# Kernel optimization log

Measured on AMD Instinct MI355X. Metric: run time of the kernel, lower is better.

Reference implementation:

```python
import jax, jax.numpy as jnp
import numpy as np

D_MODEL = 512
N_HEADS = 8
Q_SEQ_LEN = 1024
KV_SEQ_LEN = 1024
N_MODES = 64
D_HEAD = D_MODEL // N_HEADS

# FEDformer frequency_modes (deterministic/lowest branch): lowest n_modes freqs
Q_MODES = np.arange(min(N_MODES, Q_SEQ_LEN // 2))
KV_MODES = np.arange(min(N_MODES, KV_SEQ_LEN // 2))


def setup_inputs() -> dict:
    key = jax.random.key(0)
    kq, kk, kv, kwr, kwi = jax.random.split(key, 5)
    B = 8
    scale = 1.0 / (D_MODEL * D_MODEL)
    return {
        "query": jax.random.normal(kq, (B, N_HEADS, Q_SEQ_LEN, D_HEAD), jnp.float32),
        "key": jax.random.normal(kk, (B, N_HEADS, KV_SEQ_LEN, D_HEAD), jnp.float32),
        "value": jax.random.normal(kv, (B, N_HEADS, KV_SEQ_LEN, D_HEAD), jnp.float32),
        "weights_re": scale * jax.random.uniform(kwr, (N_HEADS, D_HEAD, D_HEAD, len(Q_MODES)), jnp.float32),
        "weights_im": scale * jax.random.uniform(kwi, (N_HEADS, D_HEAD, D_HEAD, len(Q_MODES)), jnp.float32),
    }


def reference(query, key, value, weights_re, weights_im):
    # value is accepted but unused by the original forward (FEA-f variant).
    B, H, L, D = query.shape
    q_modes = jnp.asarray(Q_MODES)
    kv_modes = jnp.asarray(KV_MODES)

    # [B,H,D,L] -> rfft along time -> gather selected frequency modes
    q_fft = jnp.fft.rfft(jnp.swapaxes(query, -2, -1), axis=-1)   # [B,H,D,L//2+1]
    k_fft = jnp.fft.rfft(jnp.swapaxes(key, -2, -1), axis=-1)     # [B,H,D,Lk//2+1]
    q_fft = jnp.take(q_fft, q_modes, axis=-1)                    # [B,H,D,Mq]
    k_fft = jnp.take(k_fft, kv_modes, axis=-1)                   # [B,H,D,Mk]

    # complex attention in frequency domain (no conjugation, as in torch einsum)
    scores_fft = jnp.einsum('bhdq,bhdk->bhqk', q_fft, k_fft)
    attn_fft = jnp.tanh(scores_fft)
    context_fft = jnp.einsum('bhqk,bhdk->bhdq', attn_fft, k_fft)  # [B,H,D,Mq]

    w = (weights_re + 1j * weights_im).astype(jnp.complex64)      # [H,D,D,Mq]
    context_fft = jnp.einsum('bhiq,hijq->bhjq', context_fft, w)   # [B,H,D,Mq]

    # scatter modes back into full rfft spectrum, then irfft
    out_fft = jnp.zeros((B, H, D, L // 2 + 1), jnp.complex64)
    out_fft = out_fft.at[..., q_modes].set(context_fft)
    d_model = H * D
    context = jnp.fft.irfft(out_fft / d_model / d_model, n=L, axis=-1)  # [B,H,D,L]
    return context
```

## Files before the change

### kernel.cpp

```cpp
#include <hip/hip_runtime.h>
#include <hip/hip_bf16.h>
#include <cmath>

#define BATCH 8
#define NH 8
#define BH 64
#define SEQ 1024
#define DH 64
#define NM 64

#define P_PLANE 4096
#define P_FLOATS (2*4*64*2*4096)
#define C1C_OFF  P_FLOATS
#define C2_OFF   (C1C_OFF + 64*64*64*2)

__global__ __launch_bounds__(256) void k_dft(const float* __restrict__ q,
                                             const float* __restrict__ k,
                                             float* __restrict__ P) {
  const int bid = blockIdx.x;
  const int bh = bid & 63;
  const int inp = (bid >> 6) & 1;
  const int tq = bid >> 7;
  const float* x = (inp ? k : q) + (size_t)bh * (SEQ * DH);

  __shared__ float xs[64 * 68];
  const int tid = threadIdx.x;
  const int dg = tid & 7;
  const int par = (tid >> 3) & 1;
  const int mg = tid >> 4;
  const int m0 = mg * 4, d0 = dg * 8;

  float accr[4][8] = {{0.f}}, acci[4][8] = {{0.f}};

  float stepc[4], steps[4];
#pragma unroll
  for (int mi = 0; mi < 4; ++mi) {
    float ph = (float)((m0 + mi) * 2) * (1.0f / 512.0f);
    stepc[mi] = cospif(ph);
    steps[mi] = -sinpif(ph);
  }

  for (int ch = 0; ch < 4; ++ch) {
    const int t0g = tq * 256 + ch * 64;
    const float4* src = reinterpret_cast<const float4*>(x + (size_t)t0g * DH);
#pragma unroll
    for (int i = 0; i < 4; ++i) {
      int idx = tid + i * 256;
      int tt = idx >> 4, d4 = (idx & 15) * 4;
      *reinterpret_cast<float4*>(&xs[tt * 68 + d4]) = src[idx];
    }
    __syncthreads();

    float wr[4], wi[4];
#pragma unroll
    for (int mi = 0; mi < 4; ++mi) {
      int p0 = ((m0 + mi) * (t0g + par)) & 1023;
      float ph = (float)p0 * (1.0f / 512.0f);
      wr[mi] = cospif(ph);
      wi[mi] = -sinpif(ph);
    }

#pragma unroll 4
    for (int tt = 0; tt < 32; ++tt) {
      const int t = tt * 2 + par;
      float4 a = *reinterpret_cast<const float4*>(&xs[t * 68 + d0]);
      float4 b = *reinterpret_cast<const float4*>(&xs[t * 68 + d0 + 4]);
      float xv[8] = {a.x, a.y, a.z, a.w, b.x, b.y, b.z, b.w};
#pragma unroll
      for (int mi = 0; mi < 4; ++mi) {
        float cwr = wr[mi], cwi = wi[mi];
#pragma unroll
        for (int di = 0; di < 8; ++di) {
          accr[mi][di] = fmaf(cwr, xv[di], accr[mi][di]);
          acci[mi][di] = fmaf(cwi, xv[di], acci[mi][di]);
        }
        float nr = cwr * stepc[mi] - cwi * steps[mi];
        float ni = cwr * steps[mi] + cwi * stepc[mi];
        wr[mi] = nr; wi[mi] = ni;
      }
    }
    __syncthreads();
  }

#pragma unroll
  for (int mi = 0; mi < 4; ++mi) {
#pragma unroll
    for (int di = 0; di < 8; ++di) {
      accr[mi][di] += __shfl_xor(accr[mi][di], 8, 64);
      acci[mi][di] += __shfl_xor(acci[mi][di], 8, 64);
    }
  }

  if (par == 0) {
    const size_t base = (((size_t)inp * 4 + tq) * 64 + bh) * 2 * P_PLANE;
#pragma unroll
    for (int mi = 0; mi < 4; ++mi) {
      float* pr = P + base + (size_t)(m0 + mi) * 64 + d0;
      float* pi = P + base + P_PLANE + (size_t)(m0 + mi) * 64 + d0;
      *reinterpret_cast<float4*>(pr) =
          make_float4(accr[mi][0], accr[mi][1], accr[mi][2], accr[mi][3]);
      *reinterpret_cast<float4*>(pr + 4) =
          make_float4(accr[mi][4], accr[mi][5], accr[mi][6], accr[mi][7]);
      *reinterpret_cast<float4*>(pi) =
          make_float4(acci[mi][0], acci[mi][1], acci[mi][2], acci[mi][3]);
      *reinterpret_cast<float4*>(pi + 4) =
          make_float4(acci[mi][4], acci[mi][5], acci[mi][6], acci[mi][7]);
    }
  }
}

__device__ __forceinline__ void ctanh_f(float x, float y, float& rr, float& ri) {
  float a = 2.0f * x, b = 2.0f * y;
  if (fabsf(a) > 20.0f) {
    rr = (a > 0.0f) ? 1.0f : -1.0f;
    ri = 0.0f;
  } else {
    float ea = expf(a), ena = expf(-a);
    float sb, cb;
    sincosf(b, &sb, &cb);
    float den = 0.5f * (ea + ena) + cb;
    rr = 0.5f * (ea - ena) / den;
    ri = sb / den;
  }
}

__global__ __launch_bounds__(256) void k_mid_a(const float* __restrict__ P,
                                               float* __restrict__ C1c) {
  __shared__ float Kr[64][68], Ki[64][68];
  __shared__ float Qr[8][68], Qi[8][68];
  __shared__ float Ar[8][68], Ai[8][68];
  __shared__ float C1rs[64][9], C1is[64][9];

  const int tid = threadIdx.x;
  const int bh = blockIdx.x >> 3;
  const int qo = blockIdx.x & 7;

  size_t pq[4], pk[4];
#pragma unroll
  for (int t = 0; t < 4; ++t) {
    pq[t] = (((size_t)(0 * 4 + t) * 64 + bh) * 2) * P_PLANE;
    pk[t] = (((size_t)(1 * 4 + t) * 64 + bh) * 2) * P_PLANE;
  }

  for (int idx = tid; idx < 4096; idx += 256) {
    int kk = idx >> 6, dd = idx & 63;
    float r = 0.f, im = 0.f;
#pragma unroll
    for (int t = 0; t < 4; ++t) {
      r += P[pk[t] + idx];
      im += P[pk[t] + P_PLANE + idx];
    }
    Kr[kk][dd] = r; Ki[kk][dd] = im;
  }
  for (int idx = tid; idx < 512; idx += 256) {
    int qi2 = idx >> 6, dd = idx & 63;
    int mm = qo * 8 + qi2;
    float r = 0.f, im = 0.f;
#pragma unroll
    for (int t = 0; t < 4; ++t) {
      r += P[pq[t] + mm * 64 + dd];
      im += P[pq[t] + P_PLANE + mm * 64 + dd];
    }
    Qr[qi2][dd] = r; Qi[qi2][dd] = im;
  }
  __syncthreads();

  {
    const int q = tid >> 5, k0 = tid & 31;
    float sr[2] = {0.f}, si[2] = {0.f};
    for (int d = 0; d < 64; d += 4) {
      const float4 qr = *reinterpret_cast<const float4*>(&Qr[q][d]);
      const float4 qi = *reinterpret_cast<const float4*>(&Qi[q][d]);
#pragma unroll
      for (int j = 0; j < 2; ++j) {
        const int kk = k0 + 32 * j;
        const float4 kr = *reinterpret_cast<const float4*>(&Kr[kk][d]);
        const float4 ki = *reinterpret_cast<const float4*>(&Ki[kk][d]);
        float s0 = sr[j], s1 = si[j];
        s0 = fmaf(qr.x, kr.x, s0); s0 = fmaf(-qi.x, ki.x, s0);
        s1 = fmaf(qr.x, ki.x, s1); s1 = fmaf(qi.x, kr.x, s1);
        s0 = fmaf(qr.y, kr.y, s0); s0 = fmaf(-qi.y, ki.y, s0);
        s1 = fmaf(qr.y, ki.y, s1); s1 = fmaf(qi.y, kr.y, s1);
        s0 = fmaf(qr.z, kr.z, s0); s0 = fmaf(-qi.z, ki.z, s0);
        s1 = fmaf(qr.z, ki.z, s1); s1 = fmaf(qi.z, kr.z, s1);
        s0 = fmaf(qr.w, kr.w, s0); s0 = fmaf(-qi.w, ki.w, s0);
        s1 = fmaf(qr.w, ki.w, s1); s1 = fmaf(qi.w, kr.w, s1);
        sr[j] = s0; si[j] = s1;
      }
    }
#pragma unroll
    for (int j = 0; j < 2; ++j) {
      float rr, ri;
      ctanh_f(sr[j], si[j], rr, ri);
      Ar[q][k0 + 32 * j] = rr;
      Ai[q][k0 + 32 * j] = ri;
    }
  }
  __syncthreads();

  {
    const int q = tid >> 5, d0 = (tid & 31) * 2;
    float cr[2] = {0.f}, ci[2] = {0.f};
    for (int kk = 0; kk < 64; ++kk) {
      float a_r = Ar[q][kk], a_i = Ai[q][kk];
      const float2 kr = *reinterpret_cast<const float2*>(&Kr[kk][d0]);
      const float2 ki = *reinterpret_cast<const float2*>(&Ki[kk][d0]);
      cr[0] = fmaf(a_r, kr.x, cr[0]); cr[0] = fmaf(-a_i, ki.x, cr[0]);
      ci[0] = fmaf(a_r, ki.x, ci[0]); ci[0] = fmaf(a_i, kr.x, ci[0]);
      cr[1] = fmaf(a_r, kr.y, cr[1]); cr[1] = fmaf(-a_i, ki.y, cr[1]);
      ci[1] = fmaf(a_r, ki.y, ci[1]); ci[1] = fmaf(a_i, kr.y, ci[1]);
    }
    C1rs[d0][q] = cr[0];     C1is[d0][q] = ci[0];
    C1rs[d0 + 1][q] = cr[1]; C1is[d0 + 1][q] = ci[1];
  }
  __syncthreads();

  for (int idx = tid; idx < 512; idx += 256) {
    int i = idx >> 3, ql = idx & 7;
    size_t o = (((size_t)bh * 64 + i) * 64 + qo * 8 + ql) * 2;
    *reinterpret_cast<float2*>(&C1c[o]) = make_float2(C1rs[i][ql], C1is[i][ql]);
  }
}

__global__ __launch_bounds__(64) void k_mid_b(const float* __restrict__ C1c,
                                              const float* __restrict__ wre,
                                              const float* __restrict__ wim,
                                              float* __restrict__ C2) {
  const int bid = blockIdx.x;
  const int j = bid & 63;
  const int h = (bid >> 6) & 7;
  const int bq = bid >> 9;
  const int lane = threadIdx.x;

  const int bh0 = (bq * 2 + 0) * 8 + h;
  const int bh1 = (bq * 2 + 1) * 8 + h;
  const float2* c1a = reinterpret_cast<const float2*>(C1c) + (size_t)bh0 * 4096 + lane;
  const float2* c1b = reinterpret_cast<const float2*>(C1c) + (size_t)bh1 * 4096 + lane;
  const float* wrp = wre + ((size_t)h * 4096 + j) * 64 + lane;
  const float* wip = wim + ((size_t)h * 4096 + j) * 64 + lane;

  float ar0 = 0.f, ai0 = 0.f, ar1 = 0.f, ai1 = 0.f;
#pragma unroll 8
  for (int i = 0; i < 64; ++i) {
    float wr = wrp[(size_t)i * 4096];
    float wi = wip[(size_t)i * 4096];
    float2 ca = c1a[(size_t)i * 64];
    float2 cb = c1b[(size_t)i * 64];
    ar0 = fmaf(ca.x, wr, ar0); ar0 = fmaf(-ca.y, wi, ar0);
    ai0 = fmaf(ca.x, wi, ai0); ai0 = fmaf(ca.y, wr, ai0);
    ar1 = fmaf(cb.x, wr, ar1); ar1 = fmaf(-cb.y, wi, ar1);
    ai1 = fmaf(cb.x, wi, ai1); ai1 = fmaf(cb.y, wr, ai1);
  }
  *reinterpret_cast<float2*>(&C2[(((size_t)bh0 * 64 + j) * 64 + lane) * 2]) = make_float2(ar0, ai0);
  *reinterpret_cast<float2*>(&C2[(((size_t)bh1 * 64 + j) * 64 + lane) * 2]) = make_float2(ar1, ai1);
}

__global__ __launch_bounds__(256) void k_idft(const float* __restrict__ C2,
                                              float* __restrict__ out) {
  __shared__ float Cr[64][68], Ci[64][68];
  const int tid = threadIdx.x;
  const int bh = blockIdx.x >> 3;
  const int tc = blockIdx.x & 7;
  const float s = 1.0f / (512.0f * 512.0f * 1024.0f);

  for (int idx = tid; idx < 4096; idx += 256) {
    int j = idx >> 6, m = idx & 63;
    float f = (m == 0) ? s : 2.0f * s;
    float2 c = *reinterpret_cast<const float2*>(&C2[(((size_t)bh * 64 + j) * 64 + m) * 2]);
    Cr[m][j] = f * c.x;
    Ci[m][j] = f * c.y;
  }
  __syncthreads();

  const int tg = tid & 31, jg = tid >> 5;
  const int t0 = tc * 128 + tg * 4, j0 = jg * 8;

  float sc[4], ss[4], wc[4], wsn[4];
#pragma unroll
  for (int kk = 0; kk < 4; ++kk) {
    float ph = (float)((t0 + kk) & 1023) * (1.0f / 512.0f);
    sc[kk] = cospif(ph);
    ss[kk] = sinpif(ph);
    wc[kk] = 1.0f;
    wsn[kk] = 0.0f;
  }

  float acc[4][8] = {{0.f}};
  for (int m = 0; m < 64; ++m) {
    float4 c0 = *reinterpret_cast<const float4*>(&Cr[m][j0]);
    float4 c1 = *reinterpret_cast<const float4*>(&Cr[m][j0 + 4]);
    float4 e0 = *reinterpret_cast<const float4*>(&Ci[m][j0]);
    float4 e1 = *reinterpret_cast<const float4*>(&Ci[m][j0 + 4]);
    float crv[8] = {c0.x, c0.y, c0.z, c0.w, c1.x, c1.y, c1.z, c1.w};
    float civ[8] = {e0.x, e0.y, e0.z, e0.w, e1.x, e1.y, e1.z, e1.w};
#pragma unroll
    for (int kk = 0; kk < 4; ++kk) {
      float cw = wc[kk], sw = wsn[kk];
#pragma unroll
      for (int jj = 0; jj < 8; ++jj) {
        acc[kk][jj] = fmaf(crv[jj], cw, acc[kk][jj]);
        acc[kk][jj] = fmaf(-civ[jj], sw, acc[kk][jj]);
      }
      float nr = cw * sc[kk] - sw * ss[kk];
      float ni = cw * ss[kk] + sw * sc[kk];
      wc[kk] = nr; wsn[kk] = ni;
    }
  }

#pragma unroll
  for (int jj = 0; jj < 8; ++jj) {
    *reinterpret_cast<float4*>(&out[(size_t)bh * 65536 + (size_t)(j0 + jj) * 1024 + t0]) =
        make_float4(acc[0][jj], acc[1][jj], acc[2][jj], acc[3][jj]);
  }
}

extern "C" void kernel_launch(void* const* d_in, const int* in_sizes, int n_in,
                              void* d_out, int out_size, void* d_ws, size_t ws_size,
                              hipStream_t stream) {
  const float* q   = (const float*)d_in[0];
  const float* k   = (const float*)d_in[1];
  const float* wre = (const float*)d_in[3];
  const float* wim = (const float*)d_in[4];
  float* out = (float*)d_out;
  float* ws  = (float*)d_ws;

  float* P   = ws;
  float* C1c = ws + C1C_OFF;
  float* C2  = ws + C2_OFF;

  k_dft  <<<512,  256, 0, stream>>>(q, k, P);
  k_mid_a<<<512,  256, 0, stream>>>(P, C1c);
  k_mid_b<<<2048,  64, 0, stream>>>(C1c, wre, wim, C2);
  k_idft <<<512,  256, 0, stream>>>(C2, out);
}
```

Measured before the change: 178.5 us.

## Use even/odd half-period symmetry in DFT and inverse DFT, add partial-sum reduction kernel

The forward DFT now folds x[t] and x[t+512] into their sum and difference, so even modes use the sum and odd modes use the difference. This halves the FMA work per mode, and the grid doubles to 1024 blocks, each handling one 64-sample chunk. A separate k_red kernel reduces the 8 partial results into a compact buffer, which k_mid_a then loads with float4 reads. The inverse DFT computes only half the time points and writes even+odd and even−odd to t and t+512, again halving the arithmetic. The cost is an extra kernel launch and more workspace traffic for the partials.

```diff
diff --git a/kernel.cpp b/kernel.cpp
--- a/kernel.cpp
+++ b/kernel.cpp
@@ -10,8 +10,9 @@
 #define NM 64
 
 #define P_PLANE 4096
-#define P_FLOATS (2*4*64*2*4096)
-#define C1C_OFF  P_FLOATS
+#define P_FLOATS (2*8*64*2*4096)
+#define PR_OFF   P_FLOATS
+#define C1C_OFF  (PR_OFF + 2*64*2*4096)
 #define C2_OFF   (C1C_OFF + 64*64*64*2)
 
 __global__ __launch_bounds__(256) void k_dft(const float* __restrict__ q,
@@ -23,63 +24,64 @@
   const int tq = bid >> 7;
   const float* x = (inp ? k : q) + (size_t)bh * (SEQ * DH);
 
-  __shared__ float xs[64 * 68];
+  __shared__ float se[64 * 68], so[64 * 68];
   const int tid = threadIdx.x;
   const int dg = tid & 7;
   const int par = (tid >> 3) & 1;
-  const int mg = tid >> 4;
-  const int m0 = mg * 4, d0 = dg * 8;
-
-  float accr[4][8] = {{0.f}}, acci[4][8] = {{0.f}};
-
-  float stepc[4], steps[4];
-#pragma unroll
-  for (int mi = 0; mi < 4; ++mi) {
-    float ph = (float)((m0 + mi) * 2) * (1.0f / 512.0f);
-    stepc[mi] = cospif(ph);
-    steps[mi] = -sinpif(ph);
-  }
-
-  for (int ch = 0; ch < 4; ++ch) {
-    const int t0g = tq * 256 + ch * 64;
-    const float4* src = reinterpret_cast<const float4*>(x + (size_t)t0g * DH);
+  const int pg = (tid >> 4) & 1;
+  const int mg = tid >> 5;
+  const int d0 = dg * 8;
+
+  const int t0g = tq * 64;
+  {
+    const float4* srcA = reinterpret_cast<const float4*>(x + (size_t)t0g * DH);
+    const float4* srcB = reinterpret_cast<const float4*>(x + (size_t)(t0g + 512) * DH);
 #pragma unroll
     for (int i = 0; i < 4; ++i) {
       int idx = tid + i * 256;
       int tt = idx >> 4, d4 = (idx & 15) * 4;
-      *reinterpret_cast<float4*>(&xs[tt * 68 + d4]) = src[idx];
-    }
-    __syncthreads();
-
-    float wr[4], wi[4];
+      float4 a = srcA[idx], b = srcB[idx];
+      *reinterpret_cast<float4*>(&se[tt * 68 + d4]) =
+          make_float4(a.x + b.x, a.y + b.y, a.z + b.z, a.w + b.w);
+      *reinterpret_cast<float4*>(&so[tt * 68 + d4]) =
+          make_float4(a.x - b.x, a.y - b.y, a.z - b.z, a.w - b.w);
+    }
+  }
+  __syncthreads();
+
+  const float* s = pg ? so : se;
+
+  float accr[4][8] = {{0.f}}, acci[4][8] = {{0.f}};
+  float stepc[4], steps[4], wr[4], wi[4];
+#pragma unroll
+  for (int mi = 0; mi < 4; ++mi) {
+    const int m = 2 * (mg * 4 + mi) + pg;
+    const int ps = (2 * m) & 1023;
+    stepc[mi] = cospif((float)ps * (1.0f / 512.0f));
+    steps[mi] = -sinpif((float)ps * (1.0f / 512.0f));
+    const int p0 = (m * (t0g + par)) & 1023;
+    wr[mi] = cospif((float)p0 * (1.0f / 512.0f));
+    wi[mi] = -sinpif((float)p0 * (1.0f / 512.0f));
+  }
+
+#pragma unroll 4
+  for (int k2 = 0; k2 < 32; ++k2) {
+    const int tl = 2 * k2 + par;
+    float4 a = *reinterpret_cast<const float4*>(&s[tl * 68 + d0]);
+    float4 b = *reinterpret_cast<const float4*>(&s[tl * 68 + d0 + 4]);
+    float xv[8] = {a.x, a.y, a.z, a.w, b.x, b.y, b.z, b.w};
 #pragma unroll
     for (int mi = 0; mi < 4; ++mi) {
-      int p0 = ((m0 + mi) * (t0g + par)) & 1023;
-      float ph = (float)p0 * (1.0f / 512.0f);
-      wr[mi] = cospif(ph);
-      wi[mi] = -sinpif(ph);
-    }
-
-#pragma unroll 4
-    for (int tt = 0; tt < 32; ++tt) {
-      const int t = tt * 2 + par;
-      float4 a = *reinterpret_cast<const float4*>(&xs[t * 68 + d0]);
-      float4 b = *reinterpret_cast<const float4*>(&xs[t * 68 + d0 + 4]);
-      float xv[8] = {a.x, a.y, a.z, a.w, b.x, b.y, b.z, b.w};
-#pragma unroll
-      for (int mi = 0; mi < 4; ++mi) {
-        float cwr = wr[mi], cwi = wi[mi];
-#pragma unroll
-        for (int di = 0; di < 8; ++di) {
-          accr[mi][di] = fmaf(cwr, xv[di], accr[mi][di]);
-          acci[mi][di] = fmaf(cwi, xv[di], acci[mi][di]);
-        }
-        float nr = cwr * stepc[mi] - cwi * steps[mi];
-        float ni = cwr * steps[mi] + cwi * stepc[mi];
-        wr[mi] = nr; wi[mi] = ni;
+      float cwr = wr[mi], cwi = wi[mi];
+#pragma unroll
+      for (int di = 0; di < 8; ++di) {
+        accr[mi][di] = fmaf(cwr, xv[di], accr[mi][di]);
+        acci[mi][di] = fmaf(cwi, xv[di], acci[mi][di]);
       }
-    }
-    __syncthreads();
+      float nr = cwr * stepc[mi] - cwi * steps[mi];
+      float ni = cwr * steps[mi] + cwi * stepc[mi];
+      wr[mi] = nr; wi[mi] = ni;
+    }
   }
 
 #pragma unroll
@@ -92,11 +94,12 @@
   }
 
   if (par == 0) {
-    const size_t base = (((size_t)inp * 4 + tq) * 64 + bh) * 2 * P_PLANE;
+    const size_t base = (((size_t)inp * 8 + tq) * 64 + bh) * 2 * P_PLANE;
 #pragma unroll
     for (int mi = 0; mi < 4; ++mi) {
-      float* pr = P + base + (size_t)(m0 + mi) * 64 + d0;
-      float* pi = P + base + P_PLANE + (size_t)(m0 + mi) * 64 + d0;
+      const int m = 2 * (mg * 4 + mi) + pg;
+      float* pr = P + base + (size_t)m * 64 + d0;
+      float* pi = P + base + P_PLANE + (size_t)m * 64 + d0;
       *reinterpret_cast<float4*>(pr) =
           make_float4(accr[mi][0], accr[mi][1], accr[mi][2], accr[mi][3]);
       *reinterpret_cast<float4*>(pr + 4) =
@@ -107,6 +110,22 @@
           make_float4(acci[mi][4], acci[mi][5], acci[mi][6], acci[mi][7]);
     }
   }
+}
+
+__global__ __launch_bounds__(256) void k_red(const float* __restrict__ P,
+                                             float* __restrict__ Pr) {
+  const int idx = blockIdx.x * 256 + threadIdx.x;
+  const int inp = idx >> 17;
+  const int r = idx & 131071;
+  const float4* p4 = reinterpret_cast<const float4*>(P);
+  const size_t base = ((size_t)inp * 8) * 131072 + r;
+  float4 acc = p4[base];
+#pragma unroll
+  for (int t = 1; t < 8; ++t) {
+    float4 v = p4[base + (size_t)t * 131072];
+    acc.x += v.x; acc.y += v.y; acc.z += v.z; acc.w += v.w;
+  }
+  reinterpret_cast<float4*>(Pr)[idx] = acc;
 }
 
 __device__ __forceinline__ void ctanh_f(float x, float y, float& rr, float& ri) {
@@ -124,7 +143,7 @@
   }
 }
 
-__global__ __launch_bounds__(256) void k_mid_a(const float* __restrict__ P,
+__global__ __launch_bounds__(256) void k_mid_a(const float* __restrict__ Pr,
                                                float* __restrict__ C1c) {
   __shared__ float Kr[64][68], Ki[64][68];
   __shared__ float Qr[8][68], Qi[8][68];
@@ -135,33 +154,24 @@
   const int bh = blockIdx.x >> 3;
   const int qo = blockIdx.x & 7;
 
-  size_t pq[4], pk[4];
-#pragma unroll
-  for (int t = 0; t < 4; ++t) {
-    pq[t] = (((size_t)(0 * 4 + t) * 64 + bh) * 2) * P_PLANE;
-    pk[t] = (((size_t)(1 * 4 + t) * 64 + bh) * 2) * P_PLANE;
-  }
-
-  for (int idx = tid; idx < 4096; idx += 256) {
-    int kk = idx >> 6, dd = idx & 63;
-    float r = 0.f, im = 0.f;
-#pragma unroll
-    for (int t = 0; t < 4; ++t) {
-      r += P[pk[t] + idx];
-      im += P[pk[t] + P_PLANE + idx];
-    }
-    Kr[kk][dd] = r; Ki[kk][dd] = im;
-  }
-  for (int idx = tid; idx < 512; idx += 256) {
-    int qi2 = idx >> 6, dd = idx & 63;
-    int mm = qo * 8 + qi2;
-    float r = 0.f, im = 0.f;
-#pragma unroll
-    for (int t = 0; t < 4; ++t) {
-      r += P[pq[t] + mm * 64 + dd];
-      im += P[pq[t] + P_PLANE + mm * 64 + dd];
-    }
-    Qr[qi2][dd] = r; Qi[qi2][dd] = im;
+  const float4* kbase = reinterpret_cast<const float4*>(Pr + ((size_t)(64 + bh)) * 8192);
+  for (int idx = tid; idx < 1024; idx += 256) {
+    int kk = idx >> 4, dd = (idx & 15) * 4;
+    float4 vr = kbase[idx];
+    float4 vi = kbase[idx + 1024];
+    *reinterpret_cast<float4*>(&Kr[kk][dd]) = vr;
+    *reinterpret_cast<float4*>(&Ki[kk][dd]) = vi;
+  }
+  {
+    const float4* qbase =
+        reinterpret_cast<const float4*>(Pr + (size_t)bh * 8192 + (size_t)qo * 8 * 64);
+    if (tid < 128) {
+      int qi2 = tid >> 4, dd = (tid & 15) * 4;
+      float4 vr = qbase[tid];
+      float4 vi = qbase[tid + 1024];
+      *reinterpret_cast<float4*>(&Qr[qi2][dd]) = vr;
+      *reinterpret_cast<float4*>(&Qi[qi2][dd]) = vi;
+    }
   }
   __syncthreads();
 
@@ -273,19 +283,21 @@
   __syncthreads();
 
   const int tg = tid & 31, jg = tid >> 5;
-  const int t0 = tc * 128 + tg * 4, j0 = jg * 8;
-
-  float sc[4], ss[4], wc[4], wsn[4];
-#pragma unroll
-  for (int kk = 0; kk < 4; ++kk) {
-    float ph = (float)((t0 + kk) & 1023) * (1.0f / 512.0f);
+  const int tp0 = tc * 64 + tg * 2;
+  const int j0 = jg * 8;
+
+  float sc[2], ss[2], wc[2], wsn[2];
+#pragma unroll
+  for (int kk = 0; kk < 2; ++kk) {
+    float ph = (float)((tp0 + kk) & 1023) * (1.0f / 512.0f);
     sc[kk] = cospif(ph);
     ss[kk] = sinpif(ph);
     wc[kk] = 1.0f;
     wsn[kk] = 0.0f;
   }
 
-  float acc[4][8] = {{0.f}};
+  float accE[2][8] = {{0.f}}, accO[2][8] = {{0.f}};
+#pragma unroll 2
   for (int m = 0; m < 64; ++m) {
     float4 c0 = *reinterpret_cast<const float4*>(&Cr[m][j0]);
     float4 c1 = *reinterpret_cast<const float4*>(&Cr[m][j0 + 4]);
@@ -293,8 +305,9 @@
     float4 e1 = *reinterpret_cast<const float4*>(&Ci[m][j0 + 4]);
     float crv[8] = {c0.x, c0.y, c0.z, c0.w, c1.x, c1.y, c1.z, c1.w};
     float civ[8] = {e0.x, e0.y, e0.z, e0.w, e1.x, e1.y, e1.z, e1.w};
-#pragma unroll
-    for (int kk = 0; kk < 4; ++kk) {
+    float(*acc)[8] = (m & 1) ? accO : accE;
+#pragma unroll
+    for (int kk = 0; kk < 2; ++kk) {
       float cw = wc[kk], sw = wsn[kk];
 #pragma unroll
       for (int jj = 0; jj < 8; ++jj) {
@@ -309,8 +322,11 @@
 
 #pragma unroll
   for (int jj = 0; jj < 8; ++jj) {
-    *reinterpret_cast<float4*>(&out[(size_t)bh * 65536 + (size_t)(j0 + jj) * 1024 + t0]) =
-        make_float4(acc[0][jj], acc[1][jj], acc[2][jj], acc[3][jj]);
+    float e0v = accE[0][jj], o0v = accO[0][jj];
+    float e1v = accE[1][jj], o1v = accO[1][jj];
+    float* row = &out[((size_t)bh * 64 + j0 + jj) * 1024];
+    *reinterpret_cast<float2*>(&row[tp0])       = make_float2(e0v + o0v, e1v + o1v);
+    *reinterpret_cast<float2*>(&row[tp0 + 512]) = make_float2(e0v - o0v, e1v - o1v);
   }
 }
 
@@ -325,11 +341,13 @@
   float* ws  = (float*)d_ws;
 
   float* P   = ws;
+  float* Pr  = ws + PR_OFF;
   float* C1c = ws + C1C_OFF;
   float* C2  = ws + C2_OFF;
 
-  k_dft  <<<512,  256, 0, stream>>>(q, k, P);
-  k_mid_a<<<512,  256, 0, stream>>>(P, C1c);
+  k_dft  <<<1024, 256, 0, stream>>>(q, k, P);
+  k_red  <<<1024, 256, 0, stream>>>(P, Pr);
+  k_mid_a<<<512,  256, 0, stream>>>(Pr, C1c);
   k_mid_b<<<2048,  64, 0, stream>>>(C1c, wre, wim, C2);
   k_idft <<<512,  256, 0, stream>>>(C2, out);
 }
```

Result: faster. 166.6 us (-6.6%).
